# Performance work log

Measured on AMD Instinct MI355X. Metric: run time of the kernel, lower is better.

The kernel has to match this reference:

```python
import math
import jax, jax.numpy as jnp
import numpy as np

D_MODEL = 1024
HEADS = 16
B, S = 4, 2048


def setup_inputs() -> dict:
    key = jax.random.key(0)
    ks = jax.random.split(key, 8)
    scale = 1.0 / math.sqrt(D_MODEL)
    return {
        "q": jax.random.normal(ks[0], (B, S, D_MODEL), dtype=jnp.float32),
        "k": jax.random.normal(ks[1], (B, S, D_MODEL), dtype=jnp.float32),
        "v": jax.random.normal(ks[2], (B, S, D_MODEL), dtype=jnp.float32),
        "mask": jax.random.randint(ks[3], (B, S), 0, 2).astype(jnp.bool_),
        "alibi_mask": jax.random.normal(ks[4], (1, HEADS, S, S), dtype=jnp.float32),
        "Wq": jax.random.normal(ks[5], (D_MODEL, D_MODEL), dtype=jnp.float32) * scale,
        "Wk": jax.random.normal(ks[6], (D_MODEL, D_MODEL), dtype=jnp.float32) * scale,
        "Wv": jax.random.normal(ks[7], (D_MODEL, D_MODEL), dtype=jnp.float32) * scale,
    }


def _split_heads(x):
    b, s, d = x.shape
    return x.reshape(b, s, HEADS, d // HEADS).transpose(0, 2, 1, 3)  # [B,H,S,hd]


def reference(q, k, v, mask, alibi_mask, Wq, Wk, Wv):
    # QKV projections (Linear, no bias)
    qh = _split_heads(q @ Wq)
    kh = _split_heads(k @ Wk)
    vh = _split_heads(v @ Wv)
    depth = qh.shape[-1]
    # naive full attention matrix [B,H,Sq,Sk]
    w = jnp.einsum("bhqd,bhkd->bhqk", qh, kh) / math.sqrt(depth)
    # mask: [B,Sk] -> [B,1,1,Sk], True = masked
    w = jnp.where(mask[:, None, None, :], -jnp.inf, w)
    w = w + alibi_mask
    a = jax.nn.softmax(w, axis=-1)  # dropout p=0 -> identity
    out = jnp.einsum("bhqk,bhkd->bhqd", a, vh)
    # combine heads -> [B,S,D]
    out = out.transpose(0, 2, 1, 3).reshape(q.shape[0], q.shape[1], -1)
    return (out, a)
```

## Files before the change

### kernel.cpp

```cpp
#include <hip/hip_runtime.h>
#include <hip/hip_bf16.h>
#include <math.h>

constexpr int B  = 4;
constexpr int S  = 2048;
constexpr int D  = 1024;
constexpr int H  = 16;
constexpr int HD = 64;
constexpr float LOG2E  = 1.4426950408889634f;
constexpr float SCALE2 = 0.125f * LOG2E;

using f32x4 = __attribute__((ext_vector_type(4))) float;
using s16x8 = __attribute__((ext_vector_type(8))) short;
using u16x8 = __attribute__((ext_vector_type(8))) unsigned short;
using u16x4 = __attribute__((ext_vector_type(4))) unsigned short;

__device__ __forceinline__ unsigned short f2bf(float f) {
    union { float f; unsigned u; } x; x.f = f;
    unsigned r = x.u + 0x7fffu + ((x.u >> 16) & 1u);
    return (unsigned short)(r >> 16);
}
__device__ __forceinline__ unsigned short f2bf_fast(float f) {
    union { float f; unsigned u; } x; x.f = f;
    return (unsigned short)((x.u + 0x8000u) >> 16);
}
__device__ __forceinline__ float bf2f(unsigned short h) {
    union { unsigned u; float f; } x; x.u = ((unsigned)h) << 16;
    return x.f;
}
__device__ __forceinline__ float fexp2(float x) {
#if __has_builtin(__builtin_amdgcn_exp2f)
    return __builtin_amdgcn_exp2f(x);
#else
    return __expf(x * 0.6931471805599453f);
#endif
}

#define MFMA_BF16(Af, Bf, Cf) __builtin_amdgcn_mfma_f32_16x16x32_bf16(Af, Bf, Cf, 0, 0, 0)

__global__ __launch_bounds__(256) void k_prep(
    const float* __restrict__ Xq, const float* __restrict__ Xk,
    const float* __restrict__ Xv,
    unsigned short* __restrict__ qb, unsigned short* __restrict__ kb,
    unsigned short* __restrict__ vb,
    const float* __restrict__ Wq, const float* __restrict__ Wk,
    const float* __restrict__ Wv,
    unsigned short* __restrict__ wqt, unsigned short* __restrict__ wkt,
    unsigned short* __restrict__ wvt) {
    __shared__ unsigned short T[64][68];
    const int bid = blockIdx.x;
    const int t = threadIdx.x;

    if (bid < 6144) {
        const int op = bid >> 11, xb = bid & 2047;
        const float* X = op == 0 ? Xq : (op == 1 ? Xk : Xv);
        unsigned short* O = op == 0 ? qb : (op == 1 ? kb : vb);
        const size_t N = (size_t)B * S * D;
        const size_t stride = (size_t)2048 * 256 * 8;
        for (size_t i = ((size_t)xb * 256 + t) * 8; i < N; i += stride) {
            f32x4 a0 = __builtin_nontemporal_load(reinterpret_cast<const f32x4*>(&X[i]));
            f32x4 a1 = __builtin_nontemporal_load(reinterpret_cast<const f32x4*>(&X[i + 4]));
            u16x8 o;
#pragma unroll
            for (int j = 0; j < 4; ++j) { o[j] = f2bf(a0[j]); o[4 + j] = f2bf(a1[j]); }
            *reinterpret_cast<u16x8*>(&O[i]) = o;
        }
    } else {
        const int idx = bid - 6144;
        const int op = idx >> 8, r = idx & 255;
        const float* W = op == 0 ? Wq : (op == 1 ? Wk : Wv);
        unsigned short* Wt = op == 0 ? wqt : (op == 1 ? wkt : wvt);
        const int k0 = (r & 15) * 64, n0 = (r >> 4) * 64;
        {
            const int kr = t >> 4, nc4 = (t & 15) * 4;
            for (int rr = 0; rr < 4; ++rr) {
                const int kk = kr + rr * 16;
                f32x4 wv = __builtin_nontemporal_load(
                    reinterpret_cast<const f32x4*>(&W[(size_t)(k0 + kk) * D + n0 + nc4]));
#pragma unroll
                for (int j = 0; j < 4; ++j) T[nc4 + j][kk] = f2bf(wv[j]);
            }
        }
        __syncthreads();
        {
            const int nr = t >> 4, kc4 = (t & 15) * 4;
            for (int rr = 0; rr < 4; ++rr) {
                const int nn = nr + rr * 16;
                u16x4 o;
#pragma unroll
                for (int j = 0; j < 4; ++j) o[j] = T[nn][kc4 + j];
                *reinterpret_cast<u16x4*>(&Wt[(size_t)(n0 + nn) * D + k0 + kc4]) = o;
            }
        }
    }
}

__global__ __launch_bounds__(256) void k_projabf(
    const unsigned short* __restrict__ qb, const unsigned short* __restrict__ kb,
    const unsigned short* __restrict__ vb,
    const unsigned short* __restrict__ wqt, const unsigned short* __restrict__ wkt,
    const unsigned short* __restrict__ wvt,
    unsigned short* __restrict__ qh, unsigned short* __restrict__ kh,
    unsigned short* __restrict__ vT,
    const float* __restrict__ ALIBI, unsigned short* __restrict__ ABF,
    int do_abf) {
    __shared__ alignas(16) unsigned short SM[2][128][72];
    const int bid = blockIdx.x;
    const int t = threadIdx.x;
    const int sel = bid % 11;

    if (sel < 3) {
        const int pidx = (bid / 11) * 3 + sel;
        const int op = pidx >> 10;
        const int r  = pidx & 1023;
        const int bn = (r & 7) * 128, bm = (r >> 3) * 128;
        const unsigned short* X  = op == 0 ? qb : (op == 1 ? kb : vb);
        const unsigned short* Wt = op == 0 ? wqt : (op == 1 ? wkt : wvt);
        unsigned short (*As)[72] = SM[0];
        unsigned short (*Bs)[72] = SM[1];
        const int w = t >> 6, l = t & 63;
        const int wr = w >> 1, wc = w & 1;
        const int lr = l & 15, lg = l >> 4;
        f32x4 acc[4][4] = {};

        for (int k0 = 0; k0 < D; k0 += 64) {
            for (int i = 0; i < 4; ++i) {
                const int idx = t + i * 256;
                const int row = idx >> 3, c8 = (idx & 7) * 8;
                *reinterpret_cast<u16x8*>(&As[row][c8]) =
                    *reinterpret_cast<const u16x8*>(&X[(size_t)(bm + row) * D + k0 + c8]);
                *reinterpret_cast<u16x8*>(&Bs[row][c8]) =
                    *reinterpret_cast<const u16x8*>(&Wt[(size_t)(bn + row) * D + k0 + c8]);
            }
            __syncthreads();
#pragma unroll
            for (int kk = 0; kk < 2; ++kk) {
                s16x8 af[4], bf[4];
#pragma unroll
                for (int f = 0; f < 4; ++f) {
                    af[f] = *reinterpret_cast<const s16x8*>(&As[wr * 64 + f * 16 + lr][kk * 32 + lg * 8]);
                    bf[f] = *reinterpret_cast<const s16x8*>(&Bs[wc * 64 + f * 16 + lr][kk * 32 + lg * 8]);
                }
#pragma unroll
                for (int fm = 0; fm < 4; ++fm)
#pragma unroll
                    for (int fn = 0; fn < 4; ++fn)
                        acc[fm][fn] = MFMA_BF16(af[fm], bf[fn], acc[fm][fn]);
            }
            __syncthreads();
        }

        if (op < 2) {
            unsigned short* Y = op == 0 ? qh : kh;
#pragma unroll
            for (int fm = 0; fm < 4; ++fm)
#pragma unroll
                for (int fn = 0; fn < 4; ++fn)
#pragma unroll
                    for (int rr = 0; rr < 4; ++rr) {
                        const int m = bm + wr * 64 + fm * 16 + lg * 4 + rr;
                        const int n = bn + wc * 64 + fn * 16 + lr;
                        const int b = m >> 11, s = m & (S - 1);
                        const int h = n >> 6, e = n & 63;
                        Y[(((size_t)(b * H + h) * S) + s) * HD + e] = f2bf(acc[fm][fn][rr]);
                    }
        } else {
            unsigned short (*T)[144] = reinterpret_cast<unsigned short(*)[144]>(&SM[0][0][0]);
#pragma unroll
            for (int fm = 0; fm < 4; ++fm)
#pragma unroll
                for (int fn = 0; fn < 4; ++fn)
#pragma unroll
                    for (int rr = 0; rr < 4; ++rr)
                        T[wc * 64 + fn * 16 + lr][wr * 64 + fm * 16 + lg * 4 + rr] =
                            f2bf(acc[fm][fn][rr]);
            __syncthreads();
            const int b = bm >> 11, s0 = bm & (S - 1);
            for (int it = 0; it < 8; ++it) {
                const int idx = t + it * 256;
                const int row = idx >> 4, c8 = (idx & 15) * 8;
                const int h = (bn + row) >> 6, e = (bn + row) & 63;
                *reinterpret_cast<u16x8*>(&vT[((size_t)(b * H + h) * HD + e) * S + s0 + c8]) =
                    *reinterpret_cast<const u16x8*>(&T[row][c8]);
            }
        }
    } else {
        if (!do_abf) return;
        const int aidx = (bid / 11) * 8 + (sel - 3);
        const size_t N = (size_t)H * S * S;
        const size_t stride = (size_t)8192 * 256 * 8;
        for (size_t i = ((size_t)aidx * 256 + t) * 8; i < N; i += stride) {
            f32x4 a0 = __builtin_nontemporal_load(reinterpret_cast<const f32x4*>(&ALIBI[i]));
            f32x4 a1 = __builtin_nontemporal_load(reinterpret_cast<const f32x4*>(&ALIBI[i + 4]));
            u16x8 o;
#pragma unroll
            for (int j = 0; j < 4; ++j) {
                o[j]     = f2bf(a0[j] * LOG2E);
                o[4 + j] = f2bf(a1[j] * LOG2E);
            }
            *reinterpret_cast<u16x8*>(&ABF[i]) = o;
        }
    }
}

template <bool ABF16>
__global__ __launch_bounds__(512, 4) void k_sumexp(
    const unsigned short* __restrict__ QH, const unsigned short* __restrict__ KH,
    const float* __restrict__ ALIBI, const unsigned short* __restrict__ ABF,
    const int* __restrict__ MASK, float* __restrict__ INVL) {
    __shared__ alignas(16) unsigned short Ks[64][72];
    __shared__ alignas(16) unsigned short ALs[128][72];

    const int bid = blockIdx.x;
    const int wg = (bid & 7) * 128 + (bid >> 3);
    const int bh = wg >> 4, b = bh >> 4, h = bh & 15;
    const int q0 = (wg & 15) * 128;
    const int t = threadIdx.x, w = t >> 6, ln = t & 63;
    const int lr = ln & 15, lg = ln >> 4;
    const unsigned short NEGBIG = f2bf(-1e30f);
    const size_t hoff = (size_t)h * S * S;

    const unsigned short* Kb = KH + (size_t)bh * S * HD;

    s16x8 qf[2];
#pragma unroll
    for (int kk = 0; kk < 2; ++kk)
        qf[kk] = *reinterpret_cast<const s16x8*>(
            &QH[((size_t)bh * S + q0 + w * 16 + lr) * HD + kk * 32 + lg * 8]);

    float psum = 0.f;

    for (int k0 = 0; k0 < S; k0 += 64) {
        {
            const int row = t >> 3, c8 = (t & 7) * 8;
            *reinterpret_cast<u16x8*>(&Ks[row][c8]) =
                *reinterpret_cast<const u16x8*>(&Kb[(size_t)(k0 + row) * HD + c8]);
        }
#pragma unroll
        for (int i = 0; i < 2; ++i) {
            const int idx = t + i * 512, row = idx >> 3, c8 = (idx & 7) * 8;
            int4 m0 = *reinterpret_cast<const int4*>(&MASK[b * S + k0 + c8]);
            int4 m1 = *reinterpret_cast<const int4*>(&MASK[b * S + k0 + c8 + 4]);
            u16x8 av;
            if constexpr (ABF16) {
                av = *reinterpret_cast<const u16x8*>(&ABF[hoff + (size_t)(q0 + row) * S + k0 + c8]);
            } else {
                f32x4 a0 = *reinterpret_cast<const f32x4*>(&ALIBI[hoff + (size_t)(q0 + row) * S + k0 + c8]);
                f32x4 a1 = *reinterpret_cast<const f32x4*>(&ALIBI[hoff + (size_t)(q0 + row) * S + k0 + c8 + 4]);
#pragma unroll
                for (int j = 0; j < 4; ++j) {
                    av[j] = f2bf(a0[j] * LOG2E);
                    av[4 + j] = f2bf(a1[j] * LOG2E);
                }
            }
            u16x8 sv;
            sv[0] = m0.x ? NEGBIG : av[0];
            sv[1] = m0.y ? NEGBIG : av[1];
            sv[2] = m0.z ? NEGBIG : av[2];
            sv[3] = m0.w ? NEGBIG : av[3];
            sv[4] = m1.x ? NEGBIG : av[4];
            sv[5] = m1.y ? NEGBIG : av[5];
            sv[6] = m1.z ? NEGBIG : av[6];
            sv[7] = m1.w ? NEGBIG : av[7];
            *reinterpret_cast<u16x8*>(&ALs[row][c8]) = sv;
        }
        __syncthreads();

        f32x4 acc[4] = {};
#pragma unroll
        for (int kk = 0; kk < 2; ++kk)
#pragma unroll
            for (int fn = 0; fn < 4; ++fn) {
                s16x8 kf = *reinterpret_cast<const s16x8*>(&Ks[fn * 16 + lr][kk * 32 + lg * 8]);
                acc[fn] = MFMA_BF16(kf, qf[kk], acc[fn]);
            }
#pragma unroll
        for (int fn = 0; fn < 4; ++fn) {
            u16x4 alv = *reinterpret_cast<const u16x4*>(&ALs[w * 16 + lr][fn * 16 + lg * 4]);
            f32x4 al;
#pragma unroll
            for (int j = 0; j < 4; ++j) al[j] = bf2f(alv[j]);
            f32x4 sv = acc[fn] * SCALE2 + al;
            psum += fexp2(sv[0]) + fexp2(sv[1]) + fexp2(sv[2]) + fexp2(sv[3]);
        }
        __syncthreads();
    }

    psum += __shfl_xor(psum, 16, 64);
    psum += __shfl_xor(psum, 32, 64);
    if (lg == 0)
        INVL[(size_t)bh * S + q0 + w * 16 + lr] = 1.0f / psum;
}

template <bool ABF16>
__global__ __launch_bounds__(512, 4) void k_attn(
    const unsigned short* __restrict__ QH, const unsigned short* __restrict__ KH,
    const unsigned short* __restrict__ VT, const float* __restrict__ ALIBI,
    const unsigned short* __restrict__ ABF, const int* __restrict__ MASK,
    const float* __restrict__ INVL, float* __restrict__ Aout,
    float* __restrict__ OUT) {
    __shared__ alignas(16) unsigned short Ks[64][72];
    __shared__ alignas(16) unsigned short Vs[64][72];
    __shared__ alignas(16) unsigned short ALs[128][72];

    const int bid = blockIdx.x;
    const int wg = (bid & 7) * 128 + (bid >> 3);
    const int bh = wg >> 4, b = bh >> 4, h = bh & 15;
    const int q0 = (wg & 15) * 128;
    const int t = threadIdx.x, w = t >> 6, ln = t & 63;
    const int lr = ln & 15, lg = ln >> 4;
    const unsigned short NEGBIG = f2bf(-1e30f);
    const size_t hoff = (size_t)h * S * S;

    const unsigned short* Kb = KH + (size_t)bh * S * HD;
    const unsigned short* Vb = VT + (size_t)bh * HD * S;

    s16x8 qf[2];
#pragma unroll
    for (int kk = 0; kk < 2; ++kk)
        qf[kk] = *reinterpret_cast<const s16x8*>(
            &QH[((size_t)bh * S + q0 + w * 16 + lr) * HD + kk * 32 + lg * 8]);

    const float invl = INVL[(size_t)bh * S + q0 + w * 16 + lr];
    float* arow = Aout + ((size_t)bh * S + q0 + w * 16 + lr) * S;

    f32x4 oacc[4] = {};

    for (int k0 = 0; k0 < S; k0 += 64) {
        {
            const int row = t >> 3, c8 = (t & 7) * 8;
            *reinterpret_cast<u16x8*>(&Ks[row][c8]) =
                *reinterpret_cast<const u16x8*>(&Kb[(size_t)(k0 + row) * HD + c8]);
            *reinterpret_cast<u16x8*>(&Vs[row][c8]) =
                *reinterpret_cast<const u16x8*>(&Vb[(size_t)row * S + k0 + c8]);
        }
#pragma unroll
        for (int i = 0; i < 2; ++i) {
            const int idx = t + i * 512, row = idx >> 3, c8 = (idx & 7) * 8;
            int4 m0 = *reinterpret_cast<const int4*>(&MASK[b * S + k0 + c8]);
            int4 m1 = *reinterpret_cast<const int4*>(&MASK[b * S + k0 + c8 + 4]);
            u16x8 av;
            if constexpr (ABF16) {
                av = *reinterpret_cast<const u16x8*>(&ABF[hoff + (size_t)(q0 + row) * S + k0 + c8]);
            } else {
                f32x4 a0 = *reinterpret_cast<const f32x4*>(&ALIBI[hoff + (size_t)(q0 + row) * S + k0 + c8]);
                f32x4 a1 = *reinterpret_cast<const f32x4*>(&ALIBI[hoff + (size_t)(q0 + row) * S + k0 + c8 + 4]);
#pragma unroll
                for (int j = 0; j < 4; ++j) {
                    av[j] = f2bf(a0[j] * LOG2E);
                    av[4 + j] = f2bf(a1[j] * LOG2E);
                }
            }
            u16x8 sv;
            sv[0] = m0.x ? NEGBIG : av[0];
            sv[1] = m0.y ? NEGBIG : av[1];
            sv[2] = m0.z ? NEGBIG : av[2];
            sv[3] = m0.w ? NEGBIG : av[3];
            sv[4] = m1.x ? NEGBIG : av[4];
            sv[5] = m1.y ? NEGBIG : av[5];
            sv[6] = m1.z ? NEGBIG : av[6];
            sv[7] = m1.w ? NEGBIG : av[7];
            *reinterpret_cast<u16x8*>(&ALs[row][c8]) = sv;
        }
        __syncthreads();

        f32x4 acc[4] = {};
#pragma unroll
        for (int kk = 0; kk < 2; ++kk)
#pragma unroll
            for (int fn = 0; fn < 4; ++fn) {
                s16x8 kf = *reinterpret_cast<const s16x8*>(&Ks[fn * 16 + lr][kk * 32 + lg * 8]);
                acc[fn] = MFMA_BF16(kf, qf[kk], acc[fn]);
            }

#pragma unroll
        for (int fn = 0; fn < 4; ++fn) {
            u16x4 alv = *reinterpret_cast<const u16x4*>(&ALs[w * 16 + lr][fn * 16 + lg * 4]);
            f32x4 al;
#pragma unroll
            for (int j = 0; j < 4; ++j) al[j] = bf2f(alv[j]);
            f32x4 sv = acc[fn] * SCALE2 + al;
            f32x4 p;
#pragma unroll
            for (int j = 0; j < 4; ++j) p[j] = fexp2(sv[j]);
            p *= invl;
            __builtin_nontemporal_store(
                p, reinterpret_cast<f32x4*>(arow + k0 + fn * 16 + lg * 4));
            u16x4 pb;
#pragma unroll
            for (int j = 0; j < 4; ++j) pb[j] = f2bf_fast(p[j]);
            *reinterpret_cast<u16x4*>(&ALs[w * 16 + lr][fn * 16 + lg * 4]) = pb;
        }

#pragma unroll
        for (int c = 0; c < 2; ++c) {
            s16x8 pa = *reinterpret_cast<const s16x8*>(&ALs[w * 16 + lr][c * 32 + lg * 8]);
#pragma unroll
            for (int fn = 0; fn < 4; ++fn) {
                s16x8 vf = *reinterpret_cast<const s16x8*>(&Vs[fn * 16 + lr][c * 32 + lg * 8]);
                oacc[fn] = MFMA_BF16(pa, vf, oacc[fn]);
            }
        }
        __syncthreads();
    }

#pragma unroll
    for (int fn = 0; fn < 4; ++fn)
#pragma unroll
        for (int r = 0; r < 4; ++r)
            OUT[(size_t)(b * S + q0 + w * 16 + lg * 4 + r) * D + h * HD + fn * 16 + lr] =
                oacc[fn][r];
}

extern "C" void kernel_launch(void* const* d_in, const int* in_sizes, int n_in,
                              void* d_out, int out_size, void* d_ws, size_t ws_size,
                              hipStream_t stream) {
    const float* q     = (const float*)d_in[0];
    const float* k     = (const float*)d_in[1];
    const float* v     = (const float*)d_in[2];
    const int*   mask  = (const int*)d_in[3];
    const float* alibi = (const float*)d_in[4];
    const float* Wq    = (const float*)d_in[5];
    const float* Wk    = (const float*)d_in[6];
    const float* Wv    = (const float*)d_in[7];

    float* out = (float*)d_out;
    float* a   = out + (size_t)B * S * D;

    const size_t NH = (size_t)B * H * S * HD;
    unsigned short* qh  = (unsigned short*)d_ws;
    unsigned short* kh  = qh + NH;
    unsigned short* vT  = kh + NH;
    unsigned short* wqt = vT + NH;
    unsigned short* wkt = wqt + (size_t)D * D;
    unsigned short* wvt = wkt + (size_t)D * D;
    unsigned short* qb  = wvt + (size_t)D * D;
    unsigned short* kb  = qb + NH;
    unsigned short* vb  = kb + NH;
    float*          invl = (float*)(vb + NH);
    unsigned short* abf  = (unsigned short*)(invl + (size_t)B * H * S);

    const size_t need_bf16 =
        ((size_t)(abf - qh) + (size_t)H * S * S) * sizeof(unsigned short);
    const bool use_abf16 = ws_size >= need_bf16;

    const dim3 blk(256);

    k_prep<<<dim3(6912), blk, 0, stream>>>(q, k, v, qb, kb, vb,
                                           Wq, Wk, Wv, wqt, wkt, wvt);

    k_projabf<<<dim3(11264), blk, 0, stream>>>(qb, kb, vb, wqt, wkt, wvt,
                                               qh, kh, vT, alibi, abf,
                                               use_abf16 ? 1 : 0);

    if (use_abf16) {
        k_sumexp<true><<<dim3(1024), dim3(512), 0, stream>>>(
            qh, kh, alibi, abf, mask, invl);
        k_attn<true><<<dim3(1024), dim3(512), 0, stream>>>(
            qh, kh, vT, alibi, abf, mask, invl, a, out);
    } else {
        k_sumexp<false><<<dim3(1024), dim3(512), 0, stream>>>(
            qh, kh, alibi, abf, mask, invl);
        k_attn<false><<<dim3(1024), dim3(512), 0, stream>>>(
            qh, kh, vT, alibi, abf, mask, invl, a, out);
    }
}
```

Baseline: 683.7 us.

## Move alibi bf16 conversion into prep kernel, keep projection GEMM separate

The alibi-to-bf16 conversion is moved out of the projection GEMM launch, where it was interleaved 8:3 with GEMM tiles, and into the prep kernel as extra blocks alongside the input and weight conversions. The projection GEMM becomes its own pure kernel on a 3D grid over tile column, tile row and operand. This co-schedules the purely bandwidth-bound conversions together and lets the GEMM run without competing streaming traffic. In exchange it loses the overlap of alibi streaming with GEMM compute, and the prep launch grows larger.

```diff
diff --git a/kernel.cpp b/kernel.cpp
--- a/kernel.cpp
+++ b/kernel.cpp
@@ -46,7 +46,9 @@
     const float* __restrict__ Wq, const float* __restrict__ Wk,
     const float* __restrict__ Wv,
     unsigned short* __restrict__ wqt, unsigned short* __restrict__ wkt,
-    unsigned short* __restrict__ wvt) {
+    unsigned short* __restrict__ wvt,
+    const float* __restrict__ ALIBI, unsigned short* __restrict__ ABF,
+    int do_abf) {
     __shared__ unsigned short T[64][68];
     const int bid = blockIdx.x;
     const int t = threadIdx.x;
@@ -65,7 +67,7 @@
             for (int j = 0; j < 4; ++j) { o[j] = f2bf(a0[j]); o[4 + j] = f2bf(a1[j]); }
             *reinterpret_cast<u16x8*>(&O[i]) = o;
         }
-    } else {
+    } else if (bid < 6912) {
         const int idx = bid - 6144;
         const int op = idx >> 8, r = idx & 255;
         const float* W = op == 0 ? Wq : (op == 1 ? Wk : Wv);
@@ -92,113 +94,103 @@
                 *reinterpret_cast<u16x4*>(&Wt[(size_t)(n0 + nn) * D + k0 + kc4]) = o;
             }
         }
-    }
-}
-
-__global__ __launch_bounds__(256) void k_projabf(
+    } else {
+        if (!do_abf) return;
+        const int idx = bid - 6912;
+        const size_t N = (size_t)H * S * S;
+        const size_t stride = (size_t)8192 * 256 * 8;
+        for (size_t i = ((size_t)idx * 256 + t) * 8; i < N; i += stride) {
+            f32x4 a0 = __builtin_nontemporal_load(reinterpret_cast<const f32x4*>(&ALIBI[i]));
+            f32x4 a1 = __builtin_nontemporal_load(reinterpret_cast<const f32x4*>(&ALIBI[i + 4]));
+            u16x8 o;
+#pragma unroll
+            for (int j = 0; j < 4; ++j) {
+                o[j]     = f2bf(a0[j] * LOG2E);
+                o[4 + j] = f2bf(a1[j] * LOG2E);
+            }
+            *reinterpret_cast<u16x8*>(&ABF[i]) = o;
+        }
+    }
+}
+
+__global__ __launch_bounds__(256) void k_proj3(
     const unsigned short* __restrict__ qb, const unsigned short* __restrict__ kb,
     const unsigned short* __restrict__ vb,
     const unsigned short* __restrict__ wqt, const unsigned short* __restrict__ wkt,
     const unsigned short* __restrict__ wvt,
     unsigned short* __restrict__ qh, unsigned short* __restrict__ kh,
-    unsigned short* __restrict__ vT,
-    const float* __restrict__ ALIBI, unsigned short* __restrict__ ABF,
-    int do_abf) {
+    unsigned short* __restrict__ vT) {
     __shared__ alignas(16) unsigned short SM[2][128][72];
-    const int bid = blockIdx.x;
-    const int t = threadIdx.x;
-    const int sel = bid % 11;
-
-    if (sel < 3) {
-        const int pidx = (bid / 11) * 3 + sel;
-        const int op = pidx >> 10;
-        const int r  = pidx & 1023;
-        const int bn = (r & 7) * 128, bm = (r >> 3) * 128;
-        const unsigned short* X  = op == 0 ? qb : (op == 1 ? kb : vb);
-        const unsigned short* Wt = op == 0 ? wqt : (op == 1 ? wkt : wvt);
-        unsigned short (*As)[72] = SM[0];
-        unsigned short (*Bs)[72] = SM[1];
-        const int w = t >> 6, l = t & 63;
-        const int wr = w >> 1, wc = w & 1;
-        const int lr = l & 15, lg = l >> 4;
-        f32x4 acc[4][4] = {};
-
-        for (int k0 = 0; k0 < D; k0 += 64) {
-            for (int i = 0; i < 4; ++i) {
-                const int idx = t + i * 256;
-                const int row = idx >> 3, c8 = (idx & 7) * 8;
-                *reinterpret_cast<u16x8*>(&As[row][c8]) =
-                    *reinterpret_cast<const u16x8*>(&X[(size_t)(bm + row) * D + k0 + c8]);
-                *reinterpret_cast<u16x8*>(&Bs[row][c8]) =
-                    *reinterpret_cast<const u16x8*>(&Wt[(size_t)(bn + row) * D + k0 + c8]);
-            }
-            __syncthreads();
-#pragma unroll
-            for (int kk = 0; kk < 2; ++kk) {
-                s16x8 af[4], bf[4];
-#pragma unroll
-                for (int f = 0; f < 4; ++f) {
-                    af[f] = *reinterpret_cast<const s16x8*>(&As[wr * 64 + f * 16 + lr][kk * 32 + lg * 8]);
-                    bf[f] = *reinterpret_cast<const s16x8*>(&Bs[wc * 64 + f * 16 + lr][kk * 32 + lg * 8]);
+    unsigned short (*As)[72] = SM[0];
+    unsigned short (*Bs)[72] = SM[1];
+    const int op = blockIdx.z;
+    const unsigned short* X  = op == 0 ? qb : (op == 1 ? kb : vb);
+    const unsigned short* Wt = op == 0 ? wqt : (op == 1 ? wkt : wvt);
+    const int bm = blockIdx.y * 128, bn = blockIdx.x * 128;
+    const int t = threadIdx.x, w = t >> 6, l = t & 63;
+    const int wr = w >> 1, wc = w & 1;
+    const int lr = l & 15, lg = l >> 4;
+    f32x4 acc[4][4] = {};
+
+    for (int k0 = 0; k0 < D; k0 += 64) {
+        for (int i = 0; i < 4; ++i) {
+            const int idx = t + i * 256;
+            const int row = idx >> 3, c8 = (idx & 7) * 8;
+            *reinterpret_cast<u16x8*>(&As[row][c8]) =
+                *reinterpret_cast<const u16x8*>(&X[(size_t)(bm + row) * D + k0 + c8]);
+            *reinterpret_cast<u16x8*>(&Bs[row][c8]) =
+                *reinterpret_cast<const u16x8*>(&Wt[(size_t)(bn + row) * D + k0 + c8]);
+        }
+        __syncthreads();
+#pragma unroll
+        for (int kk = 0; kk < 2; ++kk) {
+            s16x8 af[4], bf[4];
+#pragma unroll
+            for (int f = 0; f < 4; ++f) {
+                af[f] = *reinterpret_cast<const s16x8*>(&As[wr * 64 + f * 16 + lr][kk * 32 + lg * 8]);
+                bf[f] = *reinterpret_cast<const s16x8*>(&Bs[wc * 64 + f * 16 + lr][kk * 32 + lg * 8]);
+            }
+#pragma unroll
+            for (int fm = 0; fm < 4; ++fm)
+#pragma unroll
+                for (int fn = 0; fn < 4; ++fn)
+                    acc[fm][fn] = MFMA_BF16(af[fm], bf[fn], acc[fm][fn]);
+        }
+        __syncthreads();
+    }
+
+    if (op < 2) {
+        unsigned short* Y = op == 0 ? qh : kh;
+#pragma unroll
+        for (int fm = 0; fm < 4; ++fm)
+#pragma unroll
+            for (int fn = 0; fn < 4; ++fn)
+#pragma unroll
+                for (int r = 0; r < 4; ++r) {
+                    const int m = bm + wr * 64 + fm * 16 + lg * 4 + r;
+                    const int n = bn + wc * 64 + fn * 16 + lr;
+                    const int b = m >> 11, s = m & (S - 1);
+                    const int h = n >> 6, e = n & 63;
+                    Y[(((size_t)(b * H + h) * S) + s) * HD + e] = f2bf(acc[fm][fn][r]);
                 }
-#pragma unroll
-                for (int fm = 0; fm < 4; ++fm)
-#pragma unroll
-                    for (int fn = 0; fn < 4; ++fn)
-                        acc[fm][fn] = MFMA_BF16(af[fm], bf[fn], acc[fm][fn]);
-            }
-            __syncthreads();
-        }
-
-        if (op < 2) {
-            unsigned short* Y = op == 0 ? qh : kh;
-#pragma unroll
-            for (int fm = 0; fm < 4; ++fm)
-#pragma unroll
-                for (int fn = 0; fn < 4; ++fn)
-#pragma unroll
-                    for (int rr = 0; rr < 4; ++rr) {
-                        const int m = bm + wr * 64 + fm * 16 + lg * 4 + rr;
-                        const int n = bn + wc * 64 + fn * 16 + lr;
-                        const int b = m >> 11, s = m & (S - 1);
-                        const int h = n >> 6, e = n & 63;
-                        Y[(((size_t)(b * H + h) * S) + s) * HD + e] = f2bf(acc[fm][fn][rr]);
-                    }
-        } else {
-            unsigned short (*T)[144] = reinterpret_cast<unsigned short(*)[144]>(&SM[0][0][0]);
-#pragma unroll
-            for (int fm = 0; fm < 4; ++fm)
-#pragma unroll
-                for (int fn = 0; fn < 4; ++fn)
-#pragma unroll
-                    for (int rr = 0; rr < 4; ++rr)
-                        T[wc * 64 + fn * 16 + lr][wr * 64 + fm * 16 + lg * 4 + rr] =
-                            f2bf(acc[fm][fn][rr]);
-            __syncthreads();
-            const int b = bm >> 11, s0 = bm & (S - 1);
-            for (int it = 0; it < 8; ++it) {
-                const int idx = t + it * 256;
-                const int row = idx >> 4, c8 = (idx & 15) * 8;
-                const int h = (bn + row) >> 6, e = (bn + row) & 63;
-                *reinterpret_cast<u16x8*>(&vT[((size_t)(b * H + h) * HD + e) * S + s0 + c8]) =
-                    *reinterpret_cast<const u16x8*>(&T[row][c8]);
-            }
-        }
     } else {
-        if (!do_abf) return;
-        const int aidx = (bid / 11) * 8 + (sel - 3);
-        const size_t N = (size_t)H * S * S;
-        const size_t stride = (size_t)8192 * 256 * 8;
-        for (size_t i = ((size_t)aidx * 256 + t) * 8; i < N; i += stride) {
-            f32x4 a0 = __builtin_nontemporal_load(reinterpret_cast<const f32x4*>(&ALIBI[i]));
-            f32x4 a1 = __builtin_nontemporal_load(reinterpret_cast<const f32x4*>(&ALIBI[i + 4]));
-            u16x8 o;
-#pragma unroll
-            for (int j = 0; j < 4; ++j) {
-                o[j]     = f2bf(a0[j] * LOG2E);
-                o[4 + j] = f2bf(a1[j] * LOG2E);
-            }
-            *reinterpret_cast<u16x8*>(&ABF[i]) = o;
+        unsigned short (*T)[144] = reinterpret_cast<unsigned short(*)[144]>(&SM[0][0][0]);
+#pragma unroll
+        for (int fm = 0; fm < 4; ++fm)
+#pragma unroll
+            for (int fn = 0; fn < 4; ++fn)
+#pragma unroll
+                for (int r = 0; r < 4; ++r)
+                    T[wc * 64 + fn * 16 + lr][wr * 64 + fm * 16 + lg * 4 + r] =
+                        f2bf(acc[fm][fn][r]);
+        __syncthreads();
+        const int b = bm >> 11, s0 = bm & (S - 1);
+        for (int it = 0; it < 8; ++it) {
+            const int idx = t + it * 256;
+            const int row = idx >> 4, c8 = (idx & 15) * 8;
+            const int h = (bn + row) >> 6, e = (bn + row) & 63;
+            *reinterpret_cast<u16x8*>(&vT[((size_t)(b * H + h) * HD + e) * S + s0 + c8]) =
+                *reinterpret_cast<const u16x8*>(&T[row][c8]);
         }
     }
 }
@@ -446,12 +438,12 @@
 
     const dim3 blk(256);
 
-    k_prep<<<dim3(6912), blk, 0, stream>>>(q, k, v, qb, kb, vb,
-                                           Wq, Wk, Wv, wqt, wkt, wvt);
-
-    k_projabf<<<dim3(11264), blk, 0, stream>>>(qb, kb, vb, wqt, wkt, wvt,
-                                               qh, kh, vT, alibi, abf,
-                                               use_abf16 ? 1 : 0);
+    k_prep<<<dim3(15104), blk, 0, stream>>>(q, k, v, qb, kb, vb,
+                                            Wq, Wk, Wv, wqt, wkt, wvt,
+                                            alibi, abf, use_abf16 ? 1 : 0);
+
+    k_proj3<<<dim3(D / 128, (B * S) / 128, 3), blk, 0, stream>>>(
+        qb, kb, vb, wqt, wkt, wvt, qh, kh, vT);
 
     if (use_abf16) {
         k_sumexp<true><<<dim3(1024), dim3(512), 0, stream>>>(
```

Result: faster. 598.4 us (-12.5%).
